# Kernel optimization log

Hardware: AMD Instinct MI355X
Metric: run time of the kernel (lower is better)

Reference implementation:

```python
import jax, jax.numpy as jnp
from jax import lax
import numpy as np

DN = ('NCHW', 'OIHW', 'NCHW')


def _gaussian_kernel1d(ksize, sigma):
    # torchvision GaussianBlur kernel: linspace-centered, normalized pdf
    x = jnp.linspace(-(ksize - 1) * 0.5, (ksize - 1) * 0.5, ksize, dtype=jnp.float32)
    pdf = jnp.exp(-0.5 * (x / sigma) ** 2)
    return pdf / pdf.sum()


def gaussian_blur(x, ksize, sigma):
    # x: [B, 1, H, W]. Separable blur with reflect padding (== torchvision
    # GaussianBlur, whose 2D kernel is the outer product of the 1D kernel).
    k = _gaussian_kernel1d(ksize, sigma).astype(x.dtype)
    pad = ksize // 2
    xp = jnp.pad(x, ((0, 0), (0, 0), (pad, pad), (pad, pad)), mode='reflect')
    xh = lax.conv_general_dilated(xp, k.reshape(1, 1, ksize, 1), (1, 1), 'VALID',
                                  dimension_numbers=DN)
    return lax.conv_general_dilated(xh, k.reshape(1, 1, 1, ksize), (1, 1), 'VALID',
                                    dimension_numbers=DN)


def _batch_max_norm(x):
    m = jnp.max(x.reshape(x.shape[0], -1), axis=1).reshape(-1, 1, 1, 1)
    return x / m


def _batch_mean_norm(x):
    m = jnp.mean(x.reshape(x.shape[0], -1), axis=1).reshape(-1, 1, 1, 1)
    return x / m


def setup_inputs() -> dict:
    key = jax.random.key(0)
    k1, k2, k3 = jax.random.split(key, 3)
    B, C, H, W = 8, 19, 512, 512
    mask_parse = jax.random.uniform(k1, (B, C, H, W), dtype=jnp.float32)
    area_weights = jax.random.uniform(k2, (C,), dtype=jnp.float32)
    eye_shadows_weight = jax.random.uniform(k3, (1,), dtype=jnp.float32)
    return {"mask_parse": mask_parse, "area_weights": area_weights,
            "eye_shadows_weight": eye_shadows_weight}


def reference(mask_parse, area_weights, eye_shadows_weight):
    background_mask = mask_parse[:, 0:1]          # [B,1,H,W]

    def eye_weight_mask(eyes_mask):
        w = gaussian_blur(eyes_mask, 51, 15.0)
        w = w * (1.0 - eyes_mask) * (1.0 - background_mask)
        return _batch_max_norm(w)

    w_mask_l = eye_weight_mask(mask_parse[:, 4:5])
    w_mask_r = eye_weight_mask(mask_parse[:, 5:6])

    # sum_i mask_parse[:, i] * area_weights[i]
    mask = jnp.einsum('bchw,c->bhw', mask_parse, area_weights)[:, None]
    mask = mask + (w_mask_l + w_mask_r) * eye_shadows_weight
    mask = gaussian_blur(mask, 21, 2.0)
    return _batch_mean_norm(mask)
```

## Files before the change

### kernel.cpp

```cpp
#include <hip/hip_runtime.h>
#include <hip/hip_cooperative_groups.h>

namespace cg = cooperative_groups;

constexpr int B_ = 8, C_ = 19, H_ = 512, W_ = 512;
constexpr int HW_ = H_ * W_;
constexpr int NB = 512;
constexpr int NT = 512;

constexpr int LDSF    = 14880;
constexpr int A_OFF   = 14336;
constexpr int SAW_OFF = 14848;
constexpr int XH_S = 292, T2_OFF = 10512, T2_S = 292, WH_S = 260;

__device__ __forceinline__ int refl(int i, int n) {
    i = (i < 0) ? -i : i;
    return (i >= n) ? (2 * n - 2 - i) : i;
}

template<int ND>
__device__ __forceinline__ void gauss_reg(float (&wkr)[ND], float sigma) {
    float s = 0.f;
#pragma unroll
    for (int d = 0; d < ND; ++d) {
        const float t = d / sigma;
        wkr[d] = expf(-0.5f * t * t);
        s += (d ? 2.f : 1.f) * wkr[d];
    }
    const float inv = 1.f / s;
#pragma unroll
    for (int d = 0; d < ND; ++d) wkr[d] *= inv;
}

__device__ __forceinline__ float aweight(int i, const float (&wkr)[11]) {
    float a = 0.f;
#pragma unroll
    for (int t = 0; t < 21; ++t) {
        const float k = wkr[(t < 10) ? (10 - t) : (t - 10)];
        const int o = i + 10 - t;
        if (o >= 0 && o < H_) a += k;
        if (i >= 1 && i <= 10 && t <= 10 - i) a += k;
        if (i >= 501 && i <= 510 && t >= 521 - i) a += k;
    }
    return a;
}


__device__ __forceinline__ void eye_tile(const float* __restrict__ mp,
                                         float* __restrict__ t0,
                                         float* __restrict__ blockmax,
                                         float* __restrict__ eyesumw,
                                         float* lds, int tid, int vb)
{
    float kh[14];
    gauss_reg(kh, 7.5f);
    const int z = vb >> 5, ht = vb & 31;
    const int eye = z >> 3, b = z & 7;
    const int i0 = ht * 8;
    const float* sb = mp + ((long)b * C_ + 4 + eye) * HW_;

    __syncthreads();
    for (int t = 0; t < 10; ++t) {
        const int e = tid + t * NT;
        if (e < 36 * 142) {
            const int s = e / 142, p = e - s * 142;
            const int R = i0 - 14 + s;
            const long r0 = (long)refl(2 * R, H_) * W_;
            const long r1 = (long)refl(2 * R + 1, H_) * W_;
            const int fc = 4 * p - 28;
            float a0, a1;
            if (fc >= 0 && fc + 3 < W_) {
                const float4 u = *(const float4*)(sb + r0 + fc);
                const float4 v = *(const float4*)(sb + r1 + fc);
                a0 = (u.x + u.y + v.x + v.y) * 0.25f;
                a1 = (u.z + u.w + v.z + v.w) * 0.25f;
            } else {
                const int j0 = 2 * p - 14, j1 = j0 + 1;
                a0 = (sb[r0 + refl(2 * j0, W_)] + sb[r0 + refl(2 * j0 + 1, W_)]
                    + sb[r1 + refl(2 * j0, W_)] + sb[r1 + refl(2 * j0 + 1, W_)]) * 0.25f;
                a1 = (sb[r0 + refl(2 * j1, W_)] + sb[r0 + refl(2 * j1 + 1, W_)]
                    + sb[r1 + refl(2 * j1, W_)] + sb[r1 + refl(2 * j1 + 1, W_)]) * 0.25f;
            }
            lds[s * XH_S + 2 * p]     = a0;
            lds[s * XH_S + 2 * p + 1] = a1;
        }
    }
    __syncthreads();
    for (int t = 0; t < 6; ++t) {
        const int e = tid + t * NT;
        if (e < 10 * 282) {
            const int r = e / 282, oc = e - r * 282;
            float acc = 0.f;
#pragma unroll
            for (int dd = 0; dd < 27; ++dd)
                acc = fmaf(lds[(r + dd) * XH_S + oc + 1],
                           kh[(dd < 13) ? (13 - dd) : (dd - 13)], acc);
            lds[T2_OFF + r * T2_S + oc] = acc;
        }
    }
    __syncthreads();
    for (int t = 0; t < 5; ++t) {
        const int e = tid + t * NT;
        const int r = e >> 8, c = e & 255;
        float acc = 0.f;
#pragma unroll
        for (int dd = 0; dd < 27; ++dd)
            acc = fmaf(lds[T2_OFF + r * T2_S + c + dd],
                       kh[(dd < 13) ? (13 - dd) : (dd - 13)], acc);
        lds[r * WH_S + c] = acc;
    }
    __syncthreads();
    const float* A = lds + A_OFF;
    const int c = tid;
    const int j = c >> 1;
    const int jn = (c & 1) ? ((j < 255) ? j + 1 : 255) : ((j > 0) ? j - 1 : 0);
    float cv[10];
#pragma unroll
    for (int s = 0; s < 10; ++s)
        cv[s] = 0.75f * lds[s * WH_S + j] + 0.25f * lds[s * WH_S + jn];
    const float Aw = A[c];
    const long mbase = (long)b * C_ * HW_ + (long)(ht * 16) * W_ + c;
    const float* eyp = mp + mbase + (long)(4 + eye) * HW_;
    const float* bgp = mp + mbase;
    float* db = t0 + (long)z * HW_ + (long)(ht * 16) * W_ + c;
    float vmax = 0.f, vsum = 0.f;
#pragma unroll
    for (int o = 0; o < 16; ++o) {
        const int il = (o >> 1) + 1;
        const int i  = i0 + (o >> 1);
        const float cvn = (o & 1) ? ((i < 255) ? cv[il + 1] : cv[il])
                                  : ((i > 0)   ? cv[il - 1] : cv[il]);
        const float wv = 0.75f * cv[il] + 0.25f * cvn;
        const float ey = eyp[(long)o * W_], bg = bgp[(long)o * W_];
        const float v = wv * (1.f - ey) * (1.f - bg);
        db[(long)o * W_] = v;
        vmax = fmaxf(vmax, v);
        vsum = fmaf(v, A[ht * 16 + o] * Aw, vsum);
    }
#pragma unroll
    for (int off = 32; off; off >>= 1) {
        vmax = fmaxf(vmax, __shfl_down(vmax, off));
        vsum += __shfl_down(vsum, off);
    }
    __syncthreads();
    if ((tid & 63) == 0) { lds[tid >> 6] = vmax; lds[8 + (tid >> 6)] = vsum; }
    __syncthreads();
    if (tid == 0) {
        float m = lds[0], s = lds[8];
        for (int i = 1; i < 8; ++i) { m = fmaxf(m, lds[i]); s += lds[8 + i]; }
        blockmax[z * 32 + ht] = m;
        eyesumw[z * 32 + ht] = s;
    }
}

__device__ __forceinline__ void einsum_part(const float* __restrict__ mp,
                                            float* __restrict__ t3,
                                            float* __restrict__ esum,
                                            float* lds, int tid, int bid)
{
    const float* A   = lds + A_OFF;
    const float* saw = lds + SAW_OFF;
    const int b = bid >> 6, chunk = bid & 63;
    float se = 0.f;
#pragma unroll
    for (int q = 0; q < 2; ++q) {
        const int p4 = chunk * 1024 + q * 512 + tid;
        const long p = (long)p4 * 4;
        const int h = (int)(p >> 9), w0 = (int)(p & 511);
        const float* mpb = mp + (long)b * C_ * HW_ + p;
        float4 acc = make_float4(0.f, 0.f, 0.f, 0.f);
#pragma unroll
        for (int c = 0; c < C_; ++c) {
            const float4 v = *(const float4*)(mpb + (long)c * HW_);
            const float a = saw[c];
            acc.x = fmaf(v.x, a, acc.x);
            acc.y = fmaf(v.y, a, acc.y);
            acc.z = fmaf(v.z, a, acc.z);
            acc.w = fmaf(v.w, a, acc.w);
        }
        *(float4*)(t3 + (long)b * HW_ + p) = acc;
        const float dw = acc.x * A[w0] + acc.y * A[w0 + 1]
                       + acc.z * A[w0 + 2] + acc.w * A[w0 + 3];
        se = fmaf(dw, A[h], se);
    }
#pragma unroll
    for (int off = 32; off; off >>= 1) se += __shfl_down(se, off);
    __syncthreads();
    if ((tid & 63) == 0) lds[tid >> 6] = se;
    __syncthreads();
    if (tid == 0) {
        float s = 0.f;
        for (int i = 0; i < 8; ++i) s += lds[i];
        esum[bid] = s;
    }
}

__device__ __forceinline__ void phaseB(const float* __restrict__ esw,
                                       const float* __restrict__ t0,
                                       const float* __restrict__ blockmax,
                                       const float* __restrict__ eyesumw,
                                       const float* __restrict__ esum,
                                       float* __restrict__ out,
                                       float* lds, int tid, int vb)
{
    float wkr[11];
    gauss_reg(wkr, 2.f);
    const int b = vb >> 6, tile6 = vb & 63, hb = tile6 * 8;

    float mxL = blockmax[b * 32], mxR = blockmax[(8 + b) * 32];
    float SeL = 0.f, SeR = 0.f, Se = 0.f;
    for (int i = 0; i < 32; ++i) {
        mxL = fmaxf(mxL, blockmax[b * 32 + i]);
        mxR = fmaxf(mxR, blockmax[(8 + b) * 32 + i]);
        SeL += eyesumw[b * 32 + i];
        SeR += eyesumw[(8 + b) * 32 + i];
    }
    for (int i = 0; i < 64; ++i) Se += esum[b * 64 + i];
    const float e = esw[0];
    const float sl = e / mxL, sr = e / mxR;
    const float scale = (float)HW_ / (Se + sl * SeL + sr * SeR);

    const float* t1 = t0 + (long)b * HW_;
    const float* t2 = t0 + (long)(8 + b) * HW_;
    const float* t3 = t0 + (long)(16 + b) * HW_;
    float* stage = lds;
    for (int i = tid; i < 28 * 512; i += NT) {
        const int r = i >> 9, c = i & 511;
        const long off = (long)refl(hb - 10 + r, H_) * W_ + c;
        stage[i] = fmaf(t1[off], sl, fmaf(t2[off], sr, t3[off]));
    }
    __syncthreads();
    float hv[8];
#pragma unroll
    for (int j = 0; j < 8; ++j) {
        float a = 0.f;
#pragma unroll
        for (int k = 0; k < 21; ++k)
            a = fmaf(stage[(j + k) * 512 + tid], wkr[(k < 10) ? (10 - k) : (k - 10)], a);
        hv[j] = a;
    }
    __syncthreads();
#pragma unroll
    for (int j = 0; j < 8; ++j) stage[j * 512 + tid] = hv[j];
    __syncthreads();
#pragma unroll
    for (int j = 0; j < 8; ++j) {
        float a = 0.f;
#pragma unroll
        for (int k = 0; k < 21; ++k)
            a = fmaf(stage[j * 512 + refl(tid - 10 + k, W_)],
                     wkr[(k < 10) ? (10 - k) : (k - 10)], a);
        out[(long)b * HW_ + (long)(hb + j) * W_ + tid] = a * scale;
    }
}

__global__ void __launch_bounds__(NT, 4)
mega_kern(const float* __restrict__ mp, const float* __restrict__ aw,
          const float* __restrict__ esw, float* __restrict__ out,
          float* __restrict__ ws)
{
    cg::grid_group grid = cg::this_grid();
    __shared__ __align__(16) float lds[LDSF];
    const int tid = threadIdx.x, bid = blockIdx.x;
    const int vb = (bid & 7) * 64 + (bid >> 3);
    float* blockmax = ws;
    float* eyesumw  = ws + 512;
    float* esum     = ws + 1024;
    float* t0       = ws + 16384;
    float* t3       = t0 + 16L * HW_;

    {
        float w21[11];
        gauss_reg(w21, 2.f);
        lds[A_OFF + tid] = aweight(tid, w21);
    }
    if (tid < C_) lds[SAW_OFF + tid] = aw[tid];
    __syncthreads();

    if (bid & 1) {
        einsum_part(mp, t3, esum, lds, tid, bid);
        eye_tile(mp, t0, blockmax, eyesumw, lds, tid, vb);
    } else {
        eye_tile(mp, t0, blockmax, eyesumw, lds, tid, vb);
        einsum_part(mp, t3, esum, lds, tid, bid);
    }
    grid.sync();
    phaseB(esw, t0, blockmax, eyesumw, esum, out, lds, tid, vb);
}

__global__ void __launch_bounds__(NT)
fb_A_kern(const float* __restrict__ mp, const float* __restrict__ aw,
          float* __restrict__ ws)
{
    __shared__ __align__(16) float lds[LDSF];
    const int tid = threadIdx.x, bid = blockIdx.x;
    const int vb = (bid & 7) * 64 + (bid >> 3);
    float* blockmax = ws;
    float* eyesumw  = ws + 512;
    float* esum     = ws + 1024;
    float* t0       = ws + 16384;
    float* t3       = t0 + 16L * HW_;
    {
        float w21[11];
        gauss_reg(w21, 2.f);
        lds[A_OFF + tid] = aweight(tid, w21);
    }
    if (tid < C_) lds[SAW_OFF + tid] = aw[tid];
    __syncthreads();
    if (bid & 1) {
        einsum_part(mp, t3, esum, lds, tid, bid);
        eye_tile(mp, t0, blockmax, eyesumw, lds, tid, vb);
    } else {
        eye_tile(mp, t0, blockmax, eyesumw, lds, tid, vb);
        einsum_part(mp, t3, esum, lds, tid, bid);
    }
}

__global__ void __launch_bounds__(NT)
fb_B_kern(const float* __restrict__ esw, float* __restrict__ out,
          float* __restrict__ ws)
{
    __shared__ __align__(16) float lds[LDSF];
    const int tid = threadIdx.x, bid = blockIdx.x;
    const int vb = (bid & 7) * 64 + (bid >> 3);
    phaseB(esw, ws + 16384, ws, ws + 512, ws + 1024, out, lds, tid, vb);
}

extern "C" void kernel_launch(void* const* d_in, const int* in_sizes, int n_in,
                              void* d_out, int out_size, void* d_ws, size_t ws_size,
                              hipStream_t stream)
{
    const float* mp  = (const float*)d_in[0];
    const float* aw  = (const float*)d_in[1];
    const float* esw = (const float*)d_in[2];
    float* out = (float*)d_out;
    float* wsf = (float*)d_ws;

    int coop = 0, nb = 0;
    hipDeviceGetAttribute(&coop, hipDeviceAttributeCooperativeLaunch, 0);
    hipOccupancyMaxActiveBlocksPerMultiprocessor(&nb, (const void*)mega_kern, NT, 0);

    if (coop && nb >= 2) {
        void* args[] = { (void*)&mp, (void*)&aw, (void*)&esw, (void*)&out, (void*)&wsf };
        hipLaunchCooperativeKernel((void*)mega_kern, dim3(NB), dim3(NT), args, 0, stream);
    } else {
        fb_A_kern<<<NB, NT, 0, stream>>>(mp, aw, wsf);
        fb_B_kern<<<NB, NT, 0, stream>>>(esw, out, wsf);
    }
}
```

Baseline: 55.14 us.

## Register-block blur convolutions and remap block-to-work assignment for locality

Rewrites the eye-tile vertical and horizontal 27-tap passes and the phaseB 21-tap passes to load sliding windows into registers and compute several outputs per thread. This replaces repeated per-tap LDS reads with float4 loads and register reuse. PhaseB now keeps its vertical window in registers, which removes the LDS staging pass, and writes a reflect-padded row so the horizontal pass uses vectorized reads and stores. Eye and einsum work are remapped by vb so that a batch's blocks share an XCD. The cost is higher register pressure, and some threads sit idle in the eye vertical pass.

```diff
diff --git a/kernel.cpp b/kernel.cpp
--- a/kernel.cpp
+++ b/kernel.cpp
@@ -12,6 +12,7 @@
 constexpr int A_OFF   = 14336;
 constexpr int SAW_OFF = 14848;
 constexpr int XH_S = 292, T2_OFF = 10512, T2_S = 292, WH_S = 260;
+constexpr int ST_S = 540;
 
 __device__ __forceinline__ int refl(int i, int n) {
     i = (i < 0) ? -i : i;
@@ -54,8 +55,8 @@
 {
     float kh[14];
     gauss_reg(kh, 7.5f);
-    const int z = vb >> 5, ht = vb & 31;
-    const int eye = z >> 3, b = z & 7;
+    const int b = vb >> 6, eye = (vb >> 5) & 1, ht = vb & 31;
+    const int z = eye * 8 + b;
     const int i0 = ht * 8;
     const float* sb = mp + ((long)b * C_ + 4 + eye) * HW_;
 
@@ -81,33 +82,65 @@
                 a1 = (sb[r0 + refl(2 * j1, W_)] + sb[r0 + refl(2 * j1 + 1, W_)]
                     + sb[r1 + refl(2 * j1, W_)] + sb[r1 + refl(2 * j1 + 1, W_)]) * 0.25f;
             }
-            lds[s * XH_S + 2 * p]     = a0;
-            lds[s * XH_S + 2 * p + 1] = a1;
+            *(float2*)(lds + s * XH_S + 2 * p) = make_float2(a0, a1);
         }
     }
     __syncthreads();
-    for (int t = 0; t < 6; ++t) {
-        const int e = tid + t * NT;
-        if (e < 10 * 282) {
-            const int r = e / 282, oc = e - r * 282;
-            float acc = 0.f;
+    if (tid < 282) {
+        float w2[36];
+#pragma unroll
+        for (int s = 0; s < 36; ++s) w2[s] = lds[s * XH_S + tid + 1];
+#pragma unroll
+        for (int r = 0; r < 10; ++r) {
+            float a = 0.f;
 #pragma unroll
             for (int dd = 0; dd < 27; ++dd)
-                acc = fmaf(lds[(r + dd) * XH_S + oc + 1],
-                           kh[(dd < 13) ? (13 - dd) : (dd - 13)], acc);
-            lds[T2_OFF + r * T2_S + oc] = acc;
+                a = fmaf(w2[r + dd], kh[(dd < 13) ? (13 - dd) : (dd - 13)], a);
+            lds[T2_OFF + r * T2_S + tid] = a;
         }
     }
     __syncthreads();
-    for (int t = 0; t < 5; ++t) {
-        const int e = tid + t * NT;
-        const int r = e >> 8, c = e & 255;
-        float acc = 0.f;
-#pragma unroll
-        for (int dd = 0; dd < 27; ++dd)
-            acc = fmaf(lds[T2_OFF + r * T2_S + c + dd],
-                       kh[(dd < 13) ? (13 - dd) : (dd - 13)], acc);
-        lds[r * WH_S + c] = acc;
+    {
+        const int r = tid >> 6, g = tid & 63;
+        {
+            const float* trow = lds + T2_OFF + r * T2_S + 4 * g;
+            float wn[32];
+#pragma unroll
+            for (int m = 0; m < 8; ++m) {
+                const float4 v = *(const float4*)(trow + 4 * m);
+                wn[4*m] = v.x; wn[4*m+1] = v.y; wn[4*m+2] = v.z; wn[4*m+3] = v.w;
+            }
+            float o4[4];
+#pragma unroll
+            for (int o = 0; o < 4; ++o) {
+                float a = 0.f;
+#pragma unroll
+                for (int dd = 0; dd < 27; ++dd)
+                    a = fmaf(wn[o + dd], kh[(dd < 13) ? (13 - dd) : (dd - 13)], a);
+                o4[o] = a;
+            }
+            *(float4*)(lds + r * WH_S + 4 * g) = make_float4(o4[0], o4[1], o4[2], o4[3]);
+        }
+        if (tid < 128) {
+            const int r2 = 8 + (tid >> 6);
+            const float* trow = lds + T2_OFF + r2 * T2_S + 4 * g;
+            float wn[32];
+#pragma unroll
+            for (int m = 0; m < 8; ++m) {
+                const float4 v = *(const float4*)(trow + 4 * m);
+                wn[4*m] = v.x; wn[4*m+1] = v.y; wn[4*m+2] = v.z; wn[4*m+3] = v.w;
+            }
+            float o4[4];
+#pragma unroll
+            for (int o = 0; o < 4; ++o) {
+                float a = 0.f;
+#pragma unroll
+                for (int dd = 0; dd < 27; ++dd)
+                    a = fmaf(wn[o + dd], kh[(dd < 13) ? (13 - dd) : (dd - 13)], a);
+                o4[o] = a;
+            }
+            *(float4*)(lds + r2 * WH_S + 4 * g) = make_float4(o4[0], o4[1], o4[2], o4[3]);
+        }
     }
     __syncthreads();
     const float* A = lds + A_OFF;
@@ -156,11 +189,11 @@
 __device__ __forceinline__ void einsum_part(const float* __restrict__ mp,
                                             float* __restrict__ t3,
                                             float* __restrict__ esum,
-                                            float* lds, int tid, int bid)
+                                            float* lds, int tid, int vb)
 {
     const float* A   = lds + A_OFF;
     const float* saw = lds + SAW_OFF;
-    const int b = bid >> 6, chunk = bid & 63;
+    const int b = vb >> 6, chunk = vb & 63;
     float se = 0.f;
 #pragma unroll
     for (int q = 0; q < 2; ++q) {
@@ -179,9 +212,9 @@
             acc.w = fmaf(v.w, a, acc.w);
         }
         *(float4*)(t3 + (long)b * HW_ + p) = acc;
-        const float dw = acc.x * A[w0] + acc.y * A[w0 + 1]
-                       + acc.z * A[w0 + 2] + acc.w * A[w0 + 3];
-        se = fmaf(dw, A[h], se);
+        const float4 a4 = *(const float4*)(A + w0);
+        se = fmaf(acc.x * a4.x + acc.y * a4.y + acc.z * a4.z + acc.w * a4.w,
+                  A[h], se);
     }
 #pragma unroll
     for (int off = 32; off; off >>= 1) se += __shfl_down(se, off);
@@ -191,7 +224,7 @@
     if (tid == 0) {
         float s = 0.f;
         for (int i = 0; i < 8; ++i) s += lds[i];
-        esum[bid] = s;
+        esum[vb] = s;
     }
 }
 
@@ -223,35 +256,54 @@
     const float* t1 = t0 + (long)b * HW_;
     const float* t2 = t0 + (long)(8 + b) * HW_;
     const float* t3 = t0 + (long)(16 + b) * HW_;
-    float* stage = lds;
-    for (int i = tid; i < 28 * 512; i += NT) {
-        const int r = i >> 9, c = i & 511;
-        const long off = (long)refl(hb - 10 + r, H_) * W_ + c;
-        stage[i] = fmaf(t1[off], sl, fmaf(t2[off], sr, t3[off]));
-    }
-    __syncthreads();
+
+    const int c = tid;
+    float win[28];
+#pragma unroll
+    for (int i = 0; i < 28; ++i) {
+        const long off = (long)refl(hb - 10 + i, H_) * W_ + c;
+        win[i] = fmaf(t1[off], sl, fmaf(t2[off], sr, t3[off]));
+    }
     float hv[8];
 #pragma unroll
     for (int j = 0; j < 8; ++j) {
         float a = 0.f;
 #pragma unroll
         for (int k = 0; k < 21; ++k)
-            a = fmaf(stage[(j + k) * 512 + tid], wkr[(k < 10) ? (10 - k) : (k - 10)], a);
+            a = fmaf(win[j + k], wkr[(k < 10) ? (10 - k) : (k - 10)], a);
         hv[j] = a;
     }
-    __syncthreads();
-#pragma unroll
-    for (int j = 0; j < 8; ++j) stage[j * 512 + tid] = hv[j];
-    __syncthreads();
-#pragma unroll
-    for (int j = 0; j < 8; ++j) {
+    float* st = lds;
+#pragma unroll
+    for (int j = 0; j < 8; ++j) st[j * ST_S + 12 + c] = hv[j];
+    __syncthreads();
+    if (tid < 224) {
+        const int r = tid / 28, q = tid - r * 28;
+        float* srow = st + r * ST_S;
+        if (q < 12) srow[11 - q] = srow[13 + q];
+        else { const int cc = q - 12; srow[524 + cc] = srow[522 - cc]; }
+    }
+    __syncthreads();
+    const int r = tid >> 6, g = tid & 63, c0 = g * 8;
+    const float* srow = st + r * ST_S;
+    float wn[32];
+#pragma unroll
+    for (int m = 0; m < 8; ++m) {
+        const float4 v = *(const float4*)(srow + c0 + 4 * m);
+        wn[4*m] = v.x; wn[4*m+1] = v.y; wn[4*m+2] = v.z; wn[4*m+3] = v.w;
+    }
+    float oo[8];
+#pragma unroll
+    for (int o = 0; o < 8; ++o) {
         float a = 0.f;
 #pragma unroll
         for (int k = 0; k < 21; ++k)
-            a = fmaf(stage[j * 512 + refl(tid - 10 + k, W_)],
-                     wkr[(k < 10) ? (10 - k) : (k - 10)], a);
-        out[(long)b * HW_ + (long)(hb + j) * W_ + tid] = a * scale;
-    }
+            a = fmaf(wn[o + 2 + k], wkr[(k < 10) ? (10 - k) : (k - 10)], a);
+        oo[o] = a * scale;
+    }
+    float* orow = out + (long)b * HW_ + (long)(hb + r) * W_ + c0;
+    *(float4*)(orow)     = make_float4(oo[0], oo[1], oo[2], oo[3]);
+    *(float4*)(orow + 4) = make_float4(oo[4], oo[5], oo[6], oo[7]);
 }
 
 __global__ void __launch_bounds__(NT, 4)
@@ -278,11 +330,11 @@
     __syncthreads();
 
     if (bid & 1) {
-        einsum_part(mp, t3, esum, lds, tid, bid);
+        einsum_part(mp, t3, esum, lds, tid, vb);
         eye_tile(mp, t0, blockmax, eyesumw, lds, tid, vb);
     } else {
         eye_tile(mp, t0, blockmax, eyesumw, lds, tid, vb);
-        einsum_part(mp, t3, esum, lds, tid, bid);
+        einsum_part(mp, t3, esum, lds, tid, vb);
     }
     grid.sync();
     phaseB(esw, t0, blockmax, eyesumw, esum, out, lds, tid, vb);
@@ -308,11 +360,11 @@
     if (tid < C_) lds[SAW_OFF + tid] = aw[tid];
     __syncthreads();
     if (bid & 1) {
-        einsum_part(mp, t3, esum, lds, tid, bid);
+        einsum_part(mp, t3, esum, lds, tid, vb);
         eye_tile(mp, t0, blockmax, eyesumw, lds, tid, vb);
     } else {
         eye_tile(mp, t0, blockmax, eyesumw, lds, tid, vb);
-        einsum_part(mp, t3, esum, lds, tid, bid);
+        einsum_part(mp, t3, esum, lds, tid, vb);
     }
 }
 
```

New measurement: 51.51 us. 6.6% less time.
